# Performance work log

Measured on AMD Instinct MI355X. Metric: run time of the kernel, lower is better.

Reference implementation:

```python
import jax, jax.numpy as jnp
import numpy as np

BATCH, H_IMG, W_IMG = 4, 256, 512
HIDDEN, LAYERS, IN_CH = 64, 3, 3


def grid_edges(h, w):
    # torch_geometric.utils.grid: 8-connected grid + self-loops (9-point stencil).
    idx = np.arange(h * w, dtype=np.int32).reshape(h, w)
    srcs, dsts = [], []
    for dy in (-1, 0, 1):
        for dx in (-1, 0, 1):
            dst = idx[max(0, -dy):h - max(0, dy), max(0, -dx):w - max(0, dx)]
            src = idx[max(0, dy):h + min(0, dy), max(0, dx):w + min(0, dx)]
            srcs.append(src.ravel())
            dsts.append(dst.ravel())
    return np.concatenate(srcs), np.concatenate(dsts)


def setup_inputs() -> dict:
    key = jax.random.key(0)
    ks = jax.random.split(key, 8)
    src_np, dst_np = grid_edges(H_IMG, W_IMG)
    s = 0.1
    return {
        "x": jax.random.normal(ks[0], (BATCH, IN_CH, H_IMG, W_IMG), jnp.float32),
        "src": jnp.asarray(src_np, jnp.int32),
        "dst": jnp.asarray(dst_np, jnp.int32),
        "W_in": jax.random.normal(ks[1], (IN_CH, HIDDEN), jnp.float32) * s,
        "b_in": jnp.zeros((HIDDEN,), jnp.float32),
        "Wg": jax.random.normal(ks[2], (LAYERS, HIDDEN, HIDDEN), jnp.float32) * s,
        "bg": jnp.zeros((LAYERS, HIDDEN), jnp.float32),
        "W_out": jax.random.normal(ks[3], (HIDDEN, IN_CH), jnp.float32) * s,
        "b_out": jnp.zeros((IN_CH,), jnp.float32),
    }


def reference(x, src, dst, W_in, b_in, Wg, bg, W_out, b_out):
    B, C, H, W = x.shape
    N = H * W
    # [B,C,H,W] -> [B,N,C]
    xn = x.reshape(B, C, N).transpose(0, 2, 1)
    h = xn @ W_in + b_in
    # GCN symmetric normalization (all edge weights 1; self-loops already present)
    deg = jax.ops.segment_sum(jnp.ones(src.shape[0], x.dtype), dst, num_segments=N)
    dinv = jax.lax.rsqrt(jnp.maximum(deg, 1e-12))
    norm = dinv[src] * dinv[dst]  # [E]

    def aggregate(m):  # m: [E, HIDDEN] -> [N, HIDDEN]
        return jax.ops.segment_sum(m, dst, num_segments=N)

    for l in range(Wg.shape[0]):
        hl = h @ Wg[l]                              # [B,N,hd]
        msg = norm[None, :, None] * hl[:, src, :]   # gather + scale: [B,E,hd]
        agg = jax.vmap(aggregate)(msg)              # scatter-add:   [B,N,hd]
        h = jax.nn.relu(agg + bg[l])                # dropout inactive (eval mode)

    out = h @ W_out + b_out                         # [B,N,3]
    return out.transpose(0, 2, 1).reshape(B, C, H, W)
```

## Files before the change

kernel.cpp:

```cpp
#include <hip/hip_runtime.h>
#include <hip/hip_fp16.h>

#define H_IMG 256
#define W_IMG 512
#define NPIX  (H_IMG*W_IMG)
#define BATCH 4
#define HID   64

#define TX 32
#define TY 8
#define HX (TX+2)
#define HY (TY+2)
#define HN (HX*HY)
#define LTH 256


typedef _Float16 half8 __attribute__((ext_vector_type(8)));
typedef float v4f __attribute__((ext_vector_type(4)));

#define GLOAD16(gp, lp) \
  __builtin_amdgcn_global_load_lds((const __attribute__((address_space(1))) unsigned int*)(gp), \
                                   (__attribute__((address_space(3))) unsigned int*)(lp), 16, 0, 0)

__device__ __forceinline__ float dinvf(int y, int x) {
  int cy = 3 - (y==0) - (y==(H_IMG-1));
  int cx = 3 - (x==0) - (x==(W_IMG-1));
  return rsqrtf((float)(cy*cx));
}

__device__ __forceinline__ unsigned pack2(float a, float b) {
  __half2 h = __floats2half2_rn(a, b);
  return *reinterpret_cast<unsigned*>(&h);
}

__device__ __forceinline__ void fma_mix2(float& accL, float& accH, unsigned hv, float s) {
  asm("v_fma_mix_f32 %0, %2, %3, %0 op_sel:[0,0,0] op_sel_hi:[1,0,0]\n\t"
      "v_fma_mix_f32 %1, %2, %3, %1 op_sel:[1,0,0] op_sel_hi:[1,0,0]"
      : "+v"(accL), "+v"(accH)
      : "v"(hv), "v"(s));
}

__global__ void k_wg(const float* __restrict__ Wg, __half* __restrict__ WgT) {
  int idx = blockIdx.x * 256 + threadIdx.x;
  int l = idx >> 12, rem = idx & 4095;
  int f = rem >> 6, k = rem & 63;
  WgT[idx] = __float2half(Wg[(l << 12) + (k << 6) + f]);
}

__global__ void k_prep2(const __half* __restrict__ src, __half* __restrict__ dst) {
  int idx = blockIdx.x * 256 + threadIdx.x;
  if (idx < 4096) dst[idx] = src[idx];
}

template<int MODE>
__global__ __launch_bounds__(LTH, 3) void k_layer(
    const float* __restrict__ x,
    const float* __restrict__ W_in, const float* __restrict__ b_in,
    const __half* __restrict__ hin, const __half* __restrict__ wgt,
    const float* __restrict__ bg, __half* __restrict__ hout,
    const float* __restrict__ W_out, const float* __restrict__ b_out,
    float* __restrict__ outp) {
  __shared__ __half hs[HN * 64];
  const int tid = threadIdx.x;
  const int tx0 = blockIdx.x * TX;
  const int ty0 = blockIdx.y * TY;
  const int b   = blockIdx.z;

  const int l64 = tid & 63, lm = l64 & 15, lh = l64 >> 4, w = tid >> 6;

  half8 af0[4], af1[4];
  v4f cb[4];
#pragma unroll
  for (int ft = 0; ft < 4; ++ft) {
    const __half* wp = wgt + (ft*16 + lm)*64 + lh*8;
    af0[ft] = *(const half8*)wp;
    af1[ft] = *(const half8*)(wp + 32);
    cb[ft] = *(const v4f*)(bg + ft*16 + (lh << 2));
  }

  if (MODE == 0) {
    const float* xb = x + (size_t)b*3*NPIX;
    for (int n = tid; n < HN; n += LTH) {
      int row = n / HX, col = n - row*HX;
      int gy = ty0 - 1 + row, gx = tx0 - 1 + col;
      __half* hp = &hs[n << 6];
      const int s7 = n & 7;
      if ((unsigned)gy < H_IMG && (unsigned)gx < W_IMG) {
        int gi = (gy << 9) + gx;
        float x0 = xb[gi], x1 = xb[NPIX+gi], x2 = xb[2*NPIX+gi];
#pragma unroll
        for (int c8 = 0; c8 < 8; ++c8) {
          float rr[8];
#pragma unroll
          for (int k = 0; k < 8; ++k) {
            int f = (c8 << 3) + k;
            rr[k] = fmaf(x0, W_in[f], fmaf(x1, W_in[64+f], fmaf(x2, W_in[128+f], b_in[f])));
          }
          uint4 u = make_uint4(pack2(rr[0],rr[1]), pack2(rr[2],rr[3]),
                               pack2(rr[4],rr[5]), pack2(rr[6],rr[7]));
          *(uint4*)(hp + ((c8 ^ s7) << 3)) = u;
        }
      } else {
        uint4 z = make_uint4(0u,0u,0u,0u);
#pragma unroll
        for (int c8 = 0; c8 < 8; ++c8)
          *(uint4*)(hp + ((c8 ^ s7) << 3)) = z;
      }
    }
  } else {
    const __half* hb = hin + (size_t)b * NPIX * HID;
    for (int it = tid; it < HN*8; it += LTH) {
      int nl = it >> 3;
      int c8s = (it & 7) ^ (nl & 7);
      int row = nl / HX, col = nl - row*HX;
      int sy = ty0 - 1 + row, sx = tx0 - 1 + col;
      sy = max(0, min(H_IMG-1, sy));
      sx = max(0, min(W_IMG-1, sx));
      const __half* gp = hb + ((size_t)((sy << 9) + sx)) * 64 + (c8s << 3);
      GLOAD16(gp, &hs[it << 3]);
    }
  }
  __syncthreads();

  const int lx = tid & 31, ly = tid >> 5;
  const int gy = ty0 + ly, gx = tx0 + lx;
  const float dc = dinvf(gy, gx);
  float sc[9];
  int   nbn[9];
#pragma unroll
  for (int r = 0; r < 3; ++r)
#pragma unroll
    for (int c = 0; c < 3; ++c) {
      int ny = gy - 1 + r, nx = gx - 1 + c;
      bool ok = ((unsigned)ny < H_IMG) && ((unsigned)nx < W_IMG);
      sc[r*3+c] = ok ? dc * dinvf(ny, nx) : 0.f;
      nbn[r*3+c] = (ly + r)*HX + lx + c;
    }
  half8 sreg[8];
#pragma unroll
  for (int ch = 0; ch < 8; ++ch) {
    float acc[8] = {0.f,0.f,0.f,0.f,0.f,0.f,0.f,0.f};
#pragma unroll
    for (int j = 0; j < 9; ++j) {
      int nj = nbn[j];
      uint4 v = *(const uint4*)&hs[(nj << 6) + (((ch ^ (nj & 7))) << 3)];
      float s = sc[j];
      fma_mix2(acc[0], acc[1], v.x, s);
      fma_mix2(acc[2], acc[3], v.y, s);
      fma_mix2(acc[4], acc[5], v.z, s);
      fma_mix2(acc[6], acc[7], v.w, s);
    }
    half8 o;
#pragma unroll
    for (int k = 0; k < 8; ++k) o[k] = (_Float16)acc[k];
    sreg[ch] = o;
  }
  __syncthreads();

  {
    __half* hp = &hs[tid << 6];
    const int s7 = tid & 7;
#pragma unroll
    for (int ch = 0; ch < 8; ++ch)
      *(half8*)(hp + ((ch ^ s7) << 3)) = sreg[ch];
  }
  __syncthreads();

  __half* ho = (MODE != 2) ? (hout + (size_t)b * NPIX * HID) : nullptr;
#pragma unroll
  for (int i = 0; i < 4; ++i) {
    int g  = (w << 2) + i;
    int nn = (g << 4) + lm;
    const int s7 = nn & 7;
    const __half* np = &hs[nn << 6];
    half8 b0 = *(const half8*)(np + ((lh ^ s7) << 3));
    half8 b1 = *(const half8*)(np + (((lh + 4) ^ s7) << 3));
    v4f d[4];
#pragma unroll
    for (int ft = 0; ft < 4; ++ft) {
      v4f t = __builtin_amdgcn_mfma_f32_16x16x32_f16(af0[ft], b0, cb[ft], 0, 0, 0);
      d[ft]  = __builtin_amdgcn_mfma_f32_16x16x32_f16(af1[ft], b1, t,     0, 0, 0);
    }
    if (MODE != 2) {
      __half* hp = ho + (size_t)(((ty0 + (nn >> 5)) << 9) + tx0 + (nn & 31)) * HID + (lh << 2);
#pragma unroll
      for (int ft = 0; ft < 4; ++ft) {
        uint2 u;
        u.x = pack2(fmaxf(d[ft][0], 0.f), fmaxf(d[ft][1], 0.f));
        u.y = pack2(fmaxf(d[ft][2], 0.f), fmaxf(d[ft][3], 0.f));
        *(uint2*)(hp + ft*16) = u;
      }
    } else {
      __half* hp = &hs[nn << 6];
#pragma unroll
      for (int ft = 0; ft < 4; ++ft) {
        int pos = ft*16 + (lh << 2);
        int c8 = pos >> 3, sub = pos & 7;
        uint2 u;
        u.x = pack2(fmaxf(d[ft][0], 0.f), fmaxf(d[ft][1], 0.f));
        u.y = pack2(fmaxf(d[ft][2], 0.f), fmaxf(d[ft][3], 0.f));
        *(uint2*)(hp + ((c8 ^ s7) << 3) + sub) = u;
      }
    }
  }

  if (MODE == 2) {
    __syncthreads();
    const int prow = tid >> 5, pcol = tid & 31;
    const int pgi = ((ty0 + prow) << 9) + tx0 + pcol;
    const __half* hp = &hs[tid << 6];
    const int s7p = tid & 7;
    float p0 = b_out[0], p1 = b_out[1], p2 = b_out[2];
#pragma unroll
    for (int o = 0; o < 8; ++o) {
      half8 v = *(const half8*)(hp + ((o ^ s7p) << 3));
#pragma unroll
      for (int e = 0; e < 8; ++e) {
        const float* wr = W_out + (o*8 + e)*3;
        float fv = (float)v[e];
        p0 = fmaf(fv, wr[0], p0);
        p1 = fmaf(fv, wr[1], p1);
        p2 = fmaf(fv, wr[2], p2);
      }
    }
    float* ob = outp + (size_t)b*3*NPIX;
    ob[pgi] = p0; ob[NPIX + pgi] = p1; ob[2*NPIX + pgi] = p2;
  }
}

extern "C" void kernel_launch(void* const* d_in, const int* in_sizes, int n_in,
                              void* d_out, int out_size, void* d_ws, size_t ws_size,
                              hipStream_t stream) {
  const float* x     = (const float*)d_in[0];
  const float* W_in  = (const float*)d_in[3];
  const float* b_in  = (const float*)d_in[4];
  const float* Wg    = (const float*)d_in[5];
  const float* bg    = (const float*)d_in[6];
  const float* W_out = (const float*)d_in[7];
  const float* b_out = (const float*)d_in[8];
  float* out = (float*)d_out;

  __half* WgT = (__half*)d_out;
  __half* hA = (__half*)d_ws;
  __half* hB = hA + (size_t)BATCH*NPIX*HID;
  __half* w2c = hA;

  k_wg<<<dim3(48), 256, 0, stream>>>(Wg, WgT);

  dim3 lg(W_IMG/TX, H_IMG/TY, BATCH);
  k_layer<0><<<lg, LTH, 0, stream>>>(x, W_in, b_in, nullptr, WgT, bg, hA,
                                     nullptr, nullptr, nullptr);
  k_layer<1><<<lg, LTH, 0, stream>>>(nullptr, nullptr, nullptr, hA, WgT + 4096, bg + 64, hB,
                                     nullptr, nullptr, nullptr);
  k_prep2<<<dim3(16), 256, 0, stream>>>(WgT + 8192, w2c);
  k_layer<2><<<lg, LTH, 0, stream>>>(nullptr, nullptr, nullptr, hB, w2c, bg + 128, nullptr,
                                     W_out, b_out, out);
}
```

Before: 112.8 us.

## Compute stencil aggregation directly into MFMA B-operand layout for layers 0-1

```diff
diff --git a/kernel.cpp b/kernel.cpp
--- a/kernel.cpp
+++ b/kernel.cpp
@@ -22,6 +22,9 @@
   __builtin_amdgcn_global_load_lds((const __attribute__((address_space(1))) unsigned int*)(gp), \
                                    (__attribute__((address_space(3))) unsigned int*)(lp), 16, 0, 0)
 
+__device__ __forceinline__ float rs1(int v, int n) {
+  return rsqrtf((float)(3 - (v==0) - (v==(n-1))));
+}
 __device__ __forceinline__ float dinvf(int y, int x) {
   int cy = 3 - (y==0) - (y==(H_IMG-1));
   int cx = 3 - (x==0) - (x==(W_IMG-1));
@@ -122,67 +125,50 @@
   }
   __syncthreads();
 
-  const int lx = tid & 31, ly = tid >> 5;
-  const int gy = ty0 + ly, gx = tx0 + lx;
-  const float dc = dinvf(gy, gx);
-  float sc[9];
-  int   nbn[9];
-#pragma unroll
-  for (int r = 0; r < 3; ++r)
-#pragma unroll
-    for (int c = 0; c < 3; ++c) {
-      int ny = gy - 1 + r, nx = gx - 1 + c;
-      bool ok = ((unsigned)ny < H_IMG) && ((unsigned)nx < W_IMG);
-      sc[r*3+c] = ok ? dc * dinvf(ny, nx) : 0.f;
-      nbn[r*3+c] = (ly + r)*HX + lx + c;
-    }
-  half8 sreg[8];
-#pragma unroll
-  for (int ch = 0; ch < 8; ++ch) {
-    float acc[8] = {0.f,0.f,0.f,0.f,0.f,0.f,0.f,0.f};
-#pragma unroll
-    for (int j = 0; j < 9; ++j) {
-      int nj = nbn[j];
-      uint4 v = *(const uint4*)&hs[(nj << 6) + (((ch ^ (nj & 7))) << 3)];
-      float s = sc[j];
-      fma_mix2(acc[0], acc[1], v.x, s);
-      fma_mix2(acc[2], acc[3], v.y, s);
-      fma_mix2(acc[4], acc[5], v.z, s);
-      fma_mix2(acc[6], acc[7], v.w, s);
-    }
-    half8 o;
-#pragma unroll
-    for (int k = 0; k < 8; ++k) o[k] = (_Float16)acc[k];
-    sreg[ch] = o;
-  }
-  __syncthreads();
-
-  {
-    __half* hp = &hs[tid << 6];
-    const int s7 = tid & 7;
-#pragma unroll
-    for (int ch = 0; ch < 8; ++ch)
-      *(half8*)(hp + ((ch ^ s7) << 3)) = sreg[ch];
-  }
-  __syncthreads();
-
-  __half* ho = (MODE != 2) ? (hout + (size_t)b * NPIX * HID) : nullptr;
-#pragma unroll
-  for (int i = 0; i < 4; ++i) {
-    int g  = (w << 2) + i;
-    int nn = (g << 4) + lm;
-    const int s7 = nn & 7;
-    const __half* np = &hs[nn << 6];
-    half8 b0 = *(const half8*)(np + ((lh ^ s7) << 3));
-    half8 b1 = *(const half8*)(np + (((lh + 4) ^ s7) << 3));
-    v4f d[4];
-#pragma unroll
-    for (int ft = 0; ft < 4; ++ft) {
-      v4f t = __builtin_amdgcn_mfma_f32_16x16x32_f16(af0[ft], b0, cb[ft], 0, 0, 0);
-      d[ft]  = __builtin_amdgcn_mfma_f32_16x16x32_f16(af1[ft], b1, t,     0, 0, 0);
-    }
-    if (MODE != 2) {
-      __half* hp = ho + (size_t)(((ty0 + (nn >> 5)) << 9) + tx0 + (nn & 31)) * HID + (lh << 2);
+  if (MODE != 2) {
+    __half* ho = hout + (size_t)b * NPIX * HID;
+#pragma unroll
+    for (int i = 0; i < 4; ++i) {
+      const int g  = (w << 2) + i;
+      const int nn = (g << 4) + lm;
+      const int r = nn >> 5, c = nn & 31;
+      const int gy = ty0 + r, gx = tx0 + c;
+      float ry[3] = {rs1(gy-1,H_IMG), rs1(gy,H_IMG), rs1(gy+1,H_IMG)};
+      float rx[3] = {rs1(gx-1,W_IMG), rs1(gx,W_IMG), rs1(gx+1,W_IMG)};
+      const float dcc = ry[1]*rx[1];
+      float a0[8] = {0,0,0,0,0,0,0,0};
+      float a1[8] = {0,0,0,0,0,0,0,0};
+#pragma unroll
+      for (int dr = 0; dr < 3; ++dr) {
+#pragma unroll
+        for (int dx = 0; dx < 3; ++dx) {
+          int ny = gy - 1 + dr, nx = gx - 1 + dx;
+          bool ok = ((unsigned)ny < H_IMG) && ((unsigned)nx < W_IMG);
+          float s = ok ? dcc * ry[dr] * rx[dx] : 0.f;
+          int nj = (r + dr)*HX + (c + dx);
+          const __half* base = &hs[nj << 6];
+          uint4 va = *(const uint4*)(base + ((lh ^ (nj & 7)) << 3));
+          uint4 vb = *(const uint4*)(base + (((lh + 4) ^ (nj & 7)) << 3));
+          fma_mix2(a0[0], a0[1], va.x, s);
+          fma_mix2(a0[2], a0[3], va.y, s);
+          fma_mix2(a0[4], a0[5], va.z, s);
+          fma_mix2(a0[6], a0[7], va.w, s);
+          fma_mix2(a1[0], a1[1], vb.x, s);
+          fma_mix2(a1[2], a1[3], vb.y, s);
+          fma_mix2(a1[4], a1[5], vb.z, s);
+          fma_mix2(a1[6], a1[7], vb.w, s);
+        }
+      }
+      half8 b0, b1;
+#pragma unroll
+      for (int k = 0; k < 8; ++k) { b0[k] = (_Float16)a0[k]; b1[k] = (_Float16)a1[k]; }
+      v4f d[4];
+#pragma unroll
+      for (int ft = 0; ft < 4; ++ft) {
+        v4f t = __builtin_amdgcn_mfma_f32_16x16x32_f16(af0[ft], b0, cb[ft], 0, 0, 0);
+        d[ft]  = __builtin_amdgcn_mfma_f32_16x16x32_f16(af1[ft], b1, t,     0, 0, 0);
+      }
+      __half* hp = ho + (size_t)(((ty0 + r) << 9) + tx0 + c) * HID + (lh << 2);
 #pragma unroll
       for (int ft = 0; ft < 4; ++ft) {
         uint2 u;
@@ -190,7 +176,69 @@
         u.y = pack2(fmaxf(d[ft][2], 0.f), fmaxf(d[ft][3], 0.f));
         *(uint2*)(hp + ft*16) = u;
       }
-    } else {
+    }
+    return;
+  }
+
+  {
+    const int lx = tid & 31, ly = tid >> 5;
+    const int gy = ty0 + ly, gx = tx0 + lx;
+    const float dc = dinvf(gy, gx);
+    float sc[9];
+    int   nbn[9];
+#pragma unroll
+    for (int r = 0; r < 3; ++r)
+#pragma unroll
+      for (int c = 0; c < 3; ++c) {
+        int ny = gy - 1 + r, nx = gx - 1 + c;
+        bool ok = ((unsigned)ny < H_IMG) && ((unsigned)nx < W_IMG);
+        sc[r*3+c] = ok ? dc * dinvf(ny, nx) : 0.f;
+        nbn[r*3+c] = (ly + r)*HX + lx + c;
+      }
+    half8 sreg[8];
+#pragma unroll
+    for (int ch = 0; ch < 8; ++ch) {
+      float acc[8] = {0.f,0.f,0.f,0.f,0.f,0.f,0.f,0.f};
+#pragma unroll
+      for (int j = 0; j < 9; ++j) {
+        int nj = nbn[j];
+        uint4 v = *(const uint4*)&hs[(nj << 6) + (((ch ^ (nj & 7))) << 3)];
+        float s = sc[j];
+        fma_mix2(acc[0], acc[1], v.x, s);
+        fma_mix2(acc[2], acc[3], v.y, s);
+        fma_mix2(acc[4], acc[5], v.z, s);
+        fma_mix2(acc[6], acc[7], v.w, s);
+      }
+      half8 o;
+#pragma unroll
+      for (int k = 0; k < 8; ++k) o[k] = (_Float16)acc[k];
+      sreg[ch] = o;
+    }
+    __syncthreads();
+
+    {
+      __half* hp = &hs[tid << 6];
+      const int s7 = tid & 7;
+#pragma unroll
+      for (int ch = 0; ch < 8; ++ch)
+        *(half8*)(hp + ((ch ^ s7) << 3)) = sreg[ch];
+    }
+    __syncthreads();
+
+#pragma unroll
+    for (int i = 0; i < 4; ++i) {
+      int g  = (w << 2) + i;
+      int nn = (g << 4) + lm;
+      const int s7 = nn & 7;
+      const __half* np = &hs[nn << 6];
+      half8 b0 = *(const half8*)(np + ((lh ^ s7) << 3));
+      half8 b1 = *(const half8*)(np + (((lh + 4) ^ s7) << 3));
+      v4f d[4];
+#pragma unroll
+      for (int ft = 0; ft < 4; ++ft) {
+        v4f t = __builtin_amdgcn_mfma_f32_16x16x32_f16(af0[ft], b0, cb[ft], 0, 0, 0);
+        d[ft]  = __builtin_amdgcn_mfma_f32_16x16x32_f16(af1[ft], b1, t,     0, 0, 0);
+      }
       __half* hp = &hs[nn << 6];
 #pragma unroll
       for (int ft = 0; ft < 4; ++ft) {
@@ -202,9 +250,7 @@
         *(uint2*)(hp + ((c8 ^ s7) << 3) + sub) = u;
       }
     }
-  }
-
-  if (MODE == 2) {
+
     __syncthreads();
     const int prow = tid >> 5, pcol = tid & 31;
     const int pgi = ((ty0 + prow) << 9) + tx0 + pcol;
```

After: 104.2 us (median of 2 runs). -7.6%, faster.
